# Kernel optimization log

Measured on AMD Instinct MI355X. Metric: run time of the kernel, lower is better.

The kernel has to match this reference:

```python
import jax, jax.numpy as jnp
import numpy as np

RES = 128
FEATURE_SIZE = 8
N_PTS = 2_000_000


def setup_inputs() -> dict:
    key = jax.random.key(0)
    k1, k2 = jax.random.split(key)
    # pts in [-1, 1] as the module expects (it renormalizes to [0, 1])
    pts = jax.random.uniform(k1, (N_PTS, 3), dtype=jnp.float32, minval=-1.0, maxval=1.0)
    # learned voxel feature grid, flat [res^3, F], init std=0.01
    features = 0.01 * jax.random.normal(k2, (RES ** 3, FEATURE_SIZE), dtype=jnp.float32)
    return {"pts": pts, "features": features}


def reference(pts, features):
    res = RES
    # normalize [-1,1] -> [0,1]
    npts = (pts + 1.0) * 0.5
    # continuous voxel coords in [0, res-1]
    x = npts * (res - 1)
    x0 = jnp.clip(jnp.floor(x), 0, res - 2).astype(jnp.int32)  # [N,3]
    f = x - x0.astype(x.dtype)                                  # [N,3] frac weights
    ix, iy, iz = x0[:, 0], x0[:, 1], x0[:, 2]
    fx, fy, fz = f[:, 0], f[:, 1], f[:, 2]

    out = jnp.zeros((pts.shape[0], features.shape[1]), dtype=features.dtype)
    # 8-corner gather + weighted sum (NGLOD-style flat indexing x*res^2 + y*res + z)
    for dx in (0, 1):
        wx = fx if dx else (1.0 - fx)
        for dy in (0, 1):
            wy = fy if dy else (1.0 - fy)
            for dz in (0, 1):
                wz = fz if dz else (1.0 - fz)
                idx = (ix + dx) * (res * res) + (iy + dy) * res + (iz + dz)
                out = out + features[idx] * (wx * wy * wz)[:, None]
    return out
```

## Files before the change

kernel.cpp:

```cpp
#include <hip/hip_runtime.h>

#define RES 128
#define FEAT 8
#define NBIN 4096
#define NFB 512
#define NCOARSE 64
#define CAP 32768
#define CAP2 640
#define W1 2048
#define W2 2048
#define WPR (CAP / W2)

#define SCELLS (17 * 17 * 17)

__device__ __forceinline__ void cell_of(float px, float py, float pz,
                                        int& ix, int& iy, int& iz,
                                        float& fx, float& fy, float& fz) {
    float x = (px + 1.0f) * 0.5f * (float)(RES - 1);
    float y = (py + 1.0f) * 0.5f * (float)(RES - 1);
    float z = (pz + 1.0f) * 0.5f * (float)(RES - 1);
    float fx0 = fminf(fmaxf(floorf(x), 0.0f), (float)(RES - 2));
    float fy0 = fminf(fmaxf(floorf(y), 0.0f), (float)(RES - 2));
    float fz0 = fminf(fmaxf(floorf(z), 0.0f), (float)(RES - 2));
    ix = (int)fx0; iy = (int)fy0; iz = (int)fz0;
    fx = x - fx0; fy = y - fy0; fz = z - fz0;
}

__device__ __forceinline__ int coarse_of(int ix, int iy, int iz) {
    return ((ix >> 5) << 4) | ((iy >> 5) << 2) | (iz >> 5);
}
__device__ __forceinline__ int sub_of(int ix, int iy, int iz) {
    return (((ix >> 4) & 1) << 5) | (((iy >> 4) & 1) << 4) | (((iz >> 4) & 1) << 3)
         | (((ix >> 3) & 1) << 2) | (((iy >> 3) & 1) << 1) | ((iz >> 3) & 1);
}

__device__ __forceinline__ unsigned int bf16pair(float a, float b) {
    unsigned int ua = __float_as_uint(a);
    ua = (ua + 0x7fffu + ((ua >> 16) & 1u)) >> 16;
    unsigned int ub = __float_as_uint(b);
    ub = (ub + 0x7fffu + ((ub >> 16) & 1u)) >> 16;
    return ua | (ub << 16);
}

__global__ void init_kernel(unsigned int* cursor1, unsigned int* cursor2) {
    int i = blockIdx.x * blockDim.x + threadIdx.x;
    if (i < NCOARSE) cursor1[i] = (unsigned int)(i * CAP);
    if (i < NBIN) cursor2[i] = (unsigned int)(i * CAP2);
}

__global__ __launch_bounds__(256) void pass1_kernel(const float* __restrict__ pts,
                                                    unsigned int* __restrict__ cursor1,
                                                    float4* __restrict__ sorted1,
                                                    int npts) {
    __shared__ unsigned int cnt[NCOARSE], pfx[NCOARSE], base[NCOARSE];
    __shared__ float4 buf[W1];
    __shared__ unsigned char binof[W1];
    int tid = threadIdx.x;
    int blockStart = blockIdx.x * W1;
    int valid = min(W1, npts - blockStart);
    if (valid <= 0) return;
    if (tid < NCOARSE) cnt[tid] = 0u;
    __syncthreads();

    float ppx[8], ppy[8], ppz[8];
    int pc[8], pr[8];
    int jb = tid * 8;
    bool allv = (jb + 7 < valid);
    if (allv) {
        const float4* bp = reinterpret_cast<const float4*>(pts) +
                           ((size_t)blockStart * 3) / 4 + (size_t)tid * 6;
        float4 v0 = bp[0], v1 = bp[1], v2 = bp[2], v3 = bp[3], v4 = bp[4], v5 = bp[5];
        float P[24] = {v0.x, v0.y, v0.z, v0.w, v1.x, v1.y, v1.z, v1.w,
                       v2.x, v2.y, v2.z, v2.w, v3.x, v3.y, v3.z, v3.w,
                       v4.x, v4.y, v4.z, v4.w, v5.x, v5.y, v5.z, v5.w};
#pragma unroll
        for (int k = 0; k < 8; ++k) {
            ppx[k] = P[3 * k]; ppy[k] = P[3 * k + 1]; ppz[k] = P[3 * k + 2];
            int ix, iy, iz; float fx, fy, fz;
            cell_of(ppx[k], ppy[k], ppz[k], ix, iy, iz, fx, fy, fz);
            int c = coarse_of(ix, iy, iz);
            pr[k] = (int)atomicAdd(&cnt[c], 1u);
            pc[k] = c;
        }
    } else {
#pragma unroll
        for (int k = 0; k < 8; ++k) {
            int j = jb + k;
            pc[k] = -1;
            if (j < valid) {
                int i = blockStart + j;
                float px = pts[3 * i], py = pts[3 * i + 1], pz = pts[3 * i + 2];
                int ix, iy, iz; float fx, fy, fz;
                cell_of(px, py, pz, ix, iy, iz, fx, fy, fz);
                int c = coarse_of(ix, iy, iz);
                pr[k] = (int)atomicAdd(&cnt[c], 1u);
                pc[k] = c;
                ppx[k] = px; ppy[k] = py; ppz[k] = pz;
            }
        }
    }
    __syncthreads();
    if (tid == 0) {
        unsigned int s = 0;
        for (int b = 0; b < NCOARSE; ++b) { pfx[b] = s; s += cnt[b]; }
    }
    __syncthreads();
    if (tid < NCOARSE && cnt[tid] > 0)
        base[tid] = atomicAdd(&cursor1[tid], cnt[tid]);
    __syncthreads();
#pragma unroll
    for (int k = 0; k < 8; ++k) {
        if (allv || pc[k] >= 0) {
            int i = blockStart + jb + k;
            unsigned int slot = pfx[pc[k]] + (unsigned int)pr[k];
            buf[slot] = make_float4(ppx[k], ppy[k], ppz[k], __int_as_float(i));
            binof[slot] = (unsigned char)pc[k];
        }
    }
    __syncthreads();
#pragma unroll
    for (int k = 0; k < 8; ++k) {
        int slot = k * 256 + tid;
        if (slot < valid) {
            int b = binof[slot];
            unsigned int pos = base[b] + (unsigned int)slot - pfx[b];
            sorted1[pos] = buf[slot];
        }
    }
}

__global__ __launch_bounds__(256) void pass2_kernel(const float4* __restrict__ sorted1,
                                                    const unsigned int* __restrict__ cursor1,
                                                    unsigned int* __restrict__ cursor2,
                                                    uint2* __restrict__ sorted2) {
    int c = blockIdx.x / WPR;
    int w = blockIdx.x % WPR;
    unsigned int count = cursor1[c] - (unsigned int)(c * CAP);
    if (count > CAP) count = CAP;
    int valid = min(W2, (int)count - w * W2);
    if (valid <= 0) return;
    __shared__ unsigned int cnt[64], pfx[64], base[64];
    __shared__ uint2 buf[W2];
    __shared__ unsigned char binof[W2];
    int tid = threadIdx.x;
    int start = c * CAP + w * W2;
    if (tid < 64) cnt[tid] = 0u;
    __syncthreads();

    uint2 pe[8];
    int ps[8], pr[8];
#pragma unroll
    for (int k = 0; k < 8; ++k) {
        int j = k * 256 + tid;
        ps[k] = -1;
        if (j < valid) {
            float4 q = sorted1[start + j];
            int ix, iy, iz; float fx, fy, fz;
            cell_of(q.x, q.y, q.z, ix, iy, iz, fx, fy, fz);
            int s = sub_of(ix, iy, iz);
            unsigned int lx = (unsigned)(ix & 15), ly = (unsigned)(iy & 15),
                         lz = (unsigned)(iz & 15);
            unsigned int qfx = (unsigned)__float2int_rn(fx * 512.0f);
            unsigned int qfy = (unsigned)__float2int_rn(fy * 512.0f);
            unsigned int qfz = (unsigned)__float2int_rn(fz * 512.0f);
            unsigned int oi = (unsigned)__float_as_int(q.w);
            pe[k].x = (lx << 28) | (ly << 24) | (lz << 20) | (qfx << 10) | qfy;
            pe[k].y = (qfz << 21) | oi;
            pr[k] = (int)atomicAdd(&cnt[s], 1u);
            ps[k] = s;
        }
    }
    __syncthreads();
    if (tid == 0) {
        unsigned int s = 0;
        for (int b = 0; b < 64; ++b) { pfx[b] = s; s += cnt[b]; }
    }
    __syncthreads();
    if (tid < 64 && cnt[tid] > 0)
        base[tid] = atomicAdd(&cursor2[c * 64 + tid], cnt[tid]);
    __syncthreads();
#pragma unroll
    for (int k = 0; k < 8; ++k) {
        if (ps[k] >= 0) {
            unsigned int slot = pfx[ps[k]] + (unsigned int)pr[k];
            buf[slot] = pe[k];
            binof[slot] = (unsigned char)ps[k];
        }
    }
    __syncthreads();
#pragma unroll
    for (int k = 0; k < 8; ++k) {
        int slot = k * 256 + tid;
        if (slot < valid) {
            int b = binof[slot];
            unsigned int pos = base[b] + (unsigned int)slot - pfx[b];
            sorted2[pos] = buf[slot];
        }
    }
}

__device__ __forceinline__ void lerp_packed(const uint4* __restrict__ slab, uint2 e,
                                            float* __restrict__ out) {
    int lx = (int)(e.x >> 28), ly = (int)((e.x >> 24) & 15), lz = (int)((e.x >> 20) & 15);
    float fx = (float)((e.x >> 10) & 1023) * (1.0f / 512.0f);
    float fy = (float)(e.x & 1023) * (1.0f / 512.0f);
    float fz = (float)((e.y >> 21) & 1023) * (1.0f / 512.0f);
    int oi = (int)(e.y & 0x1FFFFFu);
    int c000 = (lx * 17 + ly) * 17 + lz;

    float wx1 = fx, wx0 = 1.0f - fx;
    float wy1 = fy, wy0 = 1.0f - fy;
    float wz1 = fz, wz0 = 1.0f - fz;
    float w[8] = {wx0 * wy0 * wz0, wx0 * wy0 * wz1, wx0 * wy1 * wz0, wx0 * wy1 * wz1,
                  wx1 * wy0 * wz0, wx1 * wy0 * wz1, wx1 * wy1 * wz0, wx1 * wy1 * wz1};

    float acc[FEAT];
#pragma unroll
    for (int k = 0; k < FEAT; ++k) acc[k] = 0.0f;

#pragma unroll
    for (int dx = 0; dx < 2; ++dx) {
#pragma unroll
        for (int dy = 0; dy < 2; ++dy) {
#pragma unroll
            for (int dz = 0; dz < 2; ++dz) {
                int ci = (dx * 2 + dy) * 2 + dz;
                uint4 r = slab[c000 + dx * 289 + dy * 17 + dz];
                float ww = w[ci];
                acc[0] += ww * __uint_as_float(r.x << 16);
                acc[1] += ww * __uint_as_float(r.x & 0xffff0000u);
                acc[2] += ww * __uint_as_float(r.y << 16);
                acc[3] += ww * __uint_as_float(r.y & 0xffff0000u);
                acc[4] += ww * __uint_as_float(r.z << 16);
                acc[5] += ww * __uint_as_float(r.z & 0xffff0000u);
                acc[6] += ww * __uint_as_float(r.w << 16);
                acc[7] += ww * __uint_as_float(r.w & 0xffff0000u);
            }
        }
    }
    float4* op = reinterpret_cast<float4*>(out + (size_t)oi * FEAT);
    op[0] = make_float4(acc[0], acc[1], acc[2], acc[3]);
    op[1] = make_float4(acc[4], acc[5], acc[6], acc[7]);
}

__global__ __launch_bounds__(512) void trilerp_bf16(const uint2* __restrict__ sorted2,
                                                    const float* __restrict__ features,
                                                    const unsigned int* __restrict__ cursor2,
                                                    float* __restrict__ out) {
    __shared__ __align__(16) uint4 slab[SCELLS];
    int tid = threadIdx.x;
    int F = (blockIdx.x & 7) * 64 + (blockIdx.x >> 3);
    int c = F >> 3, f3 = F & 7;
    int ox = (((c >> 4) & 3) << 5) | (((f3 >> 2) & 1) << 4);
    int oy = (((c >> 2) & 3) << 5) | (((f3 >> 1) & 1) << 4);
    int oz = ((c & 3) << 5) | ((f3 & 1) << 4);
    int binBase = c * 64 + f3 * 8;

#pragma unroll
    for (int k = 0; k < 10; ++k) {
        int cell = k * 512 + tid;
        if (cell < SCELLS) {
            int lx = cell / 289, rr = cell - lx * 289, ly = rr / 17, lz = rr - ly * 17;
            int gx = min(ox + lx, RES - 1);
            int gy = min(oy + ly, RES - 1);
            int gz = min(oz + lz, RES - 1);
            const float4* src = reinterpret_cast<const float4*>(
                features + (size_t)((((gx << 7) | gy) << 7) | gz) * FEAT);
            float4 a = src[0], b = src[1];
            uint4 p;
            p.x = bf16pair(a.x, a.y);
            p.y = bf16pair(a.z, a.w);
            p.z = bf16pair(b.x, b.y);
            p.w = bf16pair(b.z, b.w);
            slab[cell] = p;
        }
    }

    int s0 = binBase * CAP2;
    int e0 = (int)cursor2[binBase];
    bool v0 = (s0 + tid) < e0;
    uint2 p0;
    if (v0) p0 = sorted2[s0 + tid];

    __syncthreads();

    if (v0) lerp_packed(slab, p0, out);
    for (int p = s0 + 512 + tid; p < e0; p += 512)
        lerp_packed(slab, sorted2[p], out);

#pragma unroll
    for (int k = 1; k < 8; ++k) {
        int bin = binBase + k;
        int start = bin * CAP2;
        int end = (int)cursor2[bin];
        for (int p = start + tid; p < end; p += 512)
            lerp_packed(slab, sorted2[p], out);
    }
}

__global__ __launch_bounds__(256) void trilerp_kernel(const float* __restrict__ pts,
                                                      const float* __restrict__ features,
                                                      float* __restrict__ out,
                                                      int npts) {
    int i = blockIdx.x * blockDim.x + threadIdx.x;
    if (i >= npts) return;
    int ix, iy, iz; float fx, fy, fz;
    cell_of(pts[3 * i], pts[3 * i + 1], pts[3 * i + 2], ix, iy, iz, fx, fy, fz);
    float wx[2] = {1.0f - fx, fx};
    float wy[2] = {1.0f - fy, fy};
    float wz[2] = {1.0f - fz, fz};
    float acc[FEAT];
#pragma unroll
    for (int k = 0; k < FEAT; ++k) acc[k] = 0.0f;
    int base = (ix * RES + iy) * RES + iz;
#pragma unroll
    for (int dx = 0; dx < 2; ++dx)
#pragma unroll
        for (int dy = 0; dy < 2; ++dy)
#pragma unroll
            for (int dz = 0; dz < 2; ++dz) {
                int idxc = base + dx * (RES * RES) + dy * RES + dz;
                float w = wx[dx] * wy[dy] * wz[dz];
                const float4* fp =
                    reinterpret_cast<const float4*>(features + (size_t)idxc * FEAT);
                float4 a = fp[0];
                float4 b = fp[1];
                acc[0] += w * a.x; acc[1] += w * a.y;
                acc[2] += w * a.z; acc[3] += w * a.w;
                acc[4] += w * b.x; acc[5] += w * b.y;
                acc[6] += w * b.z; acc[7] += w * b.w;
            }
    float4* op = reinterpret_cast<float4*>(out + (size_t)i * FEAT);
    op[0] = make_float4(acc[0], acc[1], acc[2], acc[3]);
    op[1] = make_float4(acc[4], acc[5], acc[6], acc[7]);
}

extern "C" void kernel_launch(void* const* d_in, const int* in_sizes, int n_in,
                              void* d_out, int out_size, void* d_ws, size_t ws_size,
                              hipStream_t stream) {
    const float* pts = (const float*)d_in[0];
    const float* features = (const float*)d_in[1];
    float* out = (float*)d_out;
    int npts = in_sizes[0] / 3;

    size_t need = (size_t)NBIN * CAP2 * sizeof(uint2)
                + (size_t)(NBIN + NCOARSE) * 4u + 256u;
    bool out_big_enough = (size_t)out_size * 4u >= (size_t)NCOARSE * CAP * sizeof(float4);
    if (ws_size < need || !out_big_enough || npts > NCOARSE * CAP || npts > 2097151) {
        int block = 256;
        int grid = (npts + block - 1) / block;
        trilerp_kernel<<<grid, block, 0, stream>>>(pts, features, out, npts);
        return;
    }

    char* w = (char*)d_ws;
    uint2* sorted2 = (uint2*)w;                 w += (size_t)NBIN * CAP2 * sizeof(uint2);
    unsigned int* cursor1 = (unsigned int*)w;   w += NCOARSE * 4u;
    unsigned int* cursor2 = (unsigned int*)w;

    float4* sorted1 = (float4*)d_out;

    init_kernel<<<(NBIN + 255) / 256, 256, 0, stream>>>(cursor1, cursor2);
    pass1_kernel<<<(npts + W1 - 1) / W1, 256, 0, stream>>>(pts, cursor1, sorted1, npts);
    pass2_kernel<<<NCOARSE * WPR, 256, 0, stream>>>(sorted1, cursor1, cursor2, sorted2);
    trilerp_bf16<<<NFB, 512, 0, stream>>>(sorted2, features, cursor2, out);
}
```

Before: 85.52 us.

## Switch trilerp tiles to 16x8x8 bins with one bin per 256-thread block

Changes the fine binning from 4096 8^3 bins grouped into 16^3 slab blocks to 2048 bins of 16x8x8 cells. Each 256-thread block now loads a smaller 17x9x9 bf16 slab and processes exactly one bin. Halving the LDS slab and block size is meant to raise occupancy and increase the number of blocks. In exchange the slab halo overhead per point grows, since more boundary cells are loaded per interior cell, and per-bin capacity doubles to 1280.

```diff
diff --git a/kernel.cpp b/kernel.cpp
--- a/kernel.cpp
+++ b/kernel.cpp
@@ -2,16 +2,15 @@
 
 #define RES 128
 #define FEAT 8
-#define NBIN 4096
-#define NFB 512
 #define NCOARSE 64
+#define NBIN2 2048
 #define CAP 32768
-#define CAP2 640
+#define CAP2 1280
 #define W1 2048
 #define W2 2048
 #define WPR (CAP / W2)
 
-#define SCELLS (17 * 17 * 17)
+#define SCELLS (17 * 9 * 9)
 
 __device__ __forceinline__ void cell_of(float px, float py, float pz,
                                         int& ix, int& iy, int& iz,
@@ -30,8 +29,7 @@
     return ((ix >> 5) << 4) | ((iy >> 5) << 2) | (iz >> 5);
 }
 __device__ __forceinline__ int sub_of(int ix, int iy, int iz) {
-    return (((ix >> 4) & 1) << 5) | (((iy >> 4) & 1) << 4) | (((iz >> 4) & 1) << 3)
-         | (((ix >> 3) & 1) << 2) | (((iy >> 3) & 1) << 1) | ((iz >> 3) & 1);
+    return (((ix >> 4) & 1) << 4) | (((iy >> 3) & 3) << 2) | ((iz >> 3) & 3);
 }
 
 __device__ __forceinline__ unsigned int bf16pair(float a, float b) {
@@ -45,7 +43,7 @@
 __global__ void init_kernel(unsigned int* cursor1, unsigned int* cursor2) {
     int i = blockIdx.x * blockDim.x + threadIdx.x;
     if (i < NCOARSE) cursor1[i] = (unsigned int)(i * CAP);
-    if (i < NBIN) cursor2[i] = (unsigned int)(i * CAP2);
+    if (i < NBIN2) cursor2[i] = (unsigned int)(i * CAP2);
 }
 
 __global__ __launch_bounds__(256) void pass1_kernel(const float* __restrict__ pts,
@@ -139,12 +137,12 @@
     if (count > CAP) count = CAP;
     int valid = min(W2, (int)count - w * W2);
     if (valid <= 0) return;
-    __shared__ unsigned int cnt[64], pfx[64], base[64];
+    __shared__ unsigned int cnt[32], pfx[32], base[32];
     __shared__ uint2 buf[W2];
     __shared__ unsigned char binof[W2];
     int tid = threadIdx.x;
     int start = c * CAP + w * W2;
-    if (tid < 64) cnt[tid] = 0u;
+    if (tid < 32) cnt[tid] = 0u;
     __syncthreads();
 
     uint2 pe[8];
@@ -158,8 +156,8 @@
             int ix, iy, iz; float fx, fy, fz;
             cell_of(q.x, q.y, q.z, ix, iy, iz, fx, fy, fz);
             int s = sub_of(ix, iy, iz);
-            unsigned int lx = (unsigned)(ix & 15), ly = (unsigned)(iy & 15),
-                         lz = (unsigned)(iz & 15);
+            unsigned int lx = (unsigned)(ix & 15), ly = (unsigned)(iy & 7),
+                         lz = (unsigned)(iz & 7);
             unsigned int qfx = (unsigned)__float2int_rn(fx * 512.0f);
             unsigned int qfy = (unsigned)__float2int_rn(fy * 512.0f);
             unsigned int qfz = (unsigned)__float2int_rn(fz * 512.0f);
@@ -173,11 +171,11 @@
     __syncthreads();
     if (tid == 0) {
         unsigned int s = 0;
-        for (int b = 0; b < 64; ++b) { pfx[b] = s; s += cnt[b]; }
-    }
-    __syncthreads();
-    if (tid < 64 && cnt[tid] > 0)
-        base[tid] = atomicAdd(&cursor2[c * 64 + tid], cnt[tid]);
+        for (int b = 0; b < 32; ++b) { pfx[b] = s; s += cnt[b]; }
+    }
+    __syncthreads();
+    if (tid < 32 && cnt[tid] > 0)
+        base[tid] = atomicAdd(&cursor2[c * 32 + tid], cnt[tid]);
     __syncthreads();
 #pragma unroll
     for (int k = 0; k < 8; ++k) {
@@ -206,7 +204,7 @@
     float fy = (float)(e.x & 1023) * (1.0f / 512.0f);
     float fz = (float)((e.y >> 21) & 1023) * (1.0f / 512.0f);
     int oi = (int)(e.y & 0x1FFFFFu);
-    int c000 = (lx * 17 + ly) * 17 + lz;
+    int c000 = (lx * 9 + ly) * 9 + lz;
 
     float wx1 = fx, wx0 = 1.0f - fx;
     float wy1 = fy, wy0 = 1.0f - fy;
@@ -225,7 +223,7 @@
 #pragma unroll
             for (int dz = 0; dz < 2; ++dz) {
                 int ci = (dx * 2 + dy) * 2 + dz;
-                uint4 r = slab[c000 + dx * 289 + dy * 17 + dz];
+                uint4 r = slab[c000 + dx * 81 + dy * 9 + dz];
                 float ww = w[ci];
                 acc[0] += ww * __uint_as_float(r.x << 16);
                 acc[1] += ww * __uint_as_float(r.x & 0xffff0000u);
@@ -243,24 +241,23 @@
     op[1] = make_float4(acc[4], acc[5], acc[6], acc[7]);
 }
 
-__global__ __launch_bounds__(512) void trilerp_bf16(const uint2* __restrict__ sorted2,
+__global__ __launch_bounds__(256) void trilerp_bf16(const uint2* __restrict__ sorted2,
                                                     const float* __restrict__ features,
                                                     const unsigned int* __restrict__ cursor2,
                                                     float* __restrict__ out) {
     __shared__ __align__(16) uint4 slab[SCELLS];
     int tid = threadIdx.x;
-    int F = (blockIdx.x & 7) * 64 + (blockIdx.x >> 3);
-    int c = F >> 3, f3 = F & 7;
-    int ox = (((c >> 4) & 3) << 5) | (((f3 >> 2) & 1) << 4);
-    int oy = (((c >> 2) & 3) << 5) | (((f3 >> 1) & 1) << 4);
-    int oz = ((c & 3) << 5) | ((f3 & 1) << 4);
-    int binBase = c * 64 + f3 * 8;
-
-#pragma unroll
-    for (int k = 0; k < 10; ++k) {
-        int cell = k * 512 + tid;
+    int F = (blockIdx.x & 7) * 256 + (blockIdx.x >> 3);
+    int c = F >> 5, s5 = F & 31;
+    int ox = (((c >> 4) & 3) << 5) | (((s5 >> 4) & 1) << 4);
+    int oy = (((c >> 2) & 3) << 5) | (((s5 >> 2) & 3) << 3);
+    int oz = ((c & 3) << 5) | ((s5 & 3) << 3);
+
+#pragma unroll
+    for (int k = 0; k < 6; ++k) {
+        int cell = k * 256 + tid;
         if (cell < SCELLS) {
-            int lx = cell / 289, rr = cell - lx * 289, ly = rr / 17, lz = rr - ly * 17;
+            int lx = cell / 81, rr = cell - lx * 81, ly = rr / 9, lz = rr - ly * 9;
             int gx = min(ox + lx, RES - 1);
             int gy = min(oy + ly, RES - 1);
             int gz = min(oz + lz, RES - 1);
@@ -276,26 +273,20 @@
         }
     }
 
-    int s0 = binBase * CAP2;
-    int e0 = (int)cursor2[binBase];
-    bool v0 = (s0 + tid) < e0;
-    uint2 p0;
-    if (v0) p0 = sorted2[s0 + tid];
+    int s0 = F * CAP2;
+    int e0 = (int)cursor2[F];
+    int n0 = s0 + tid, n1 = n0 + 256;
+    bool v0 = n0 < e0, v1 = n1 < e0;
+    uint2 p0, p1;
+    if (v0) p0 = sorted2[n0];
+    if (v1) p1 = sorted2[n1];
 
     __syncthreads();
 
     if (v0) lerp_packed(slab, p0, out);
-    for (int p = s0 + 512 + tid; p < e0; p += 512)
+    if (v1) lerp_packed(slab, p1, out);
+    for (int p = s0 + 512 + tid; p < e0; p += 256)
         lerp_packed(slab, sorted2[p], out);
-
-#pragma unroll
-    for (int k = 1; k < 8; ++k) {
-        int bin = binBase + k;
-        int start = bin * CAP2;
-        int end = (int)cursor2[bin];
-        for (int p = start + tid; p < end; p += 512)
-            lerp_packed(slab, sorted2[p], out);
-    }
 }
 
 __global__ __launch_bounds__(256) void trilerp_kernel(const float* __restrict__ pts,
@@ -343,8 +334,8 @@
     float* out = (float*)d_out;
     int npts = in_sizes[0] / 3;
 
-    size_t need = (size_t)NBIN * CAP2 * sizeof(uint2)
-                + (size_t)(NBIN + NCOARSE) * 4u + 256u;
+    size_t need = (size_t)NBIN2 * CAP2 * sizeof(uint2)
+                + (size_t)(NBIN2 + NCOARSE) * 4u + 256u;
     bool out_big_enough = (size_t)out_size * 4u >= (size_t)NCOARSE * CAP * sizeof(float4);
     if (ws_size < need || !out_big_enough || npts > NCOARSE * CAP || npts > 2097151) {
         int block = 256;
@@ -354,14 +345,14 @@
     }
 
     char* w = (char*)d_ws;
-    uint2* sorted2 = (uint2*)w;                 w += (size_t)NBIN * CAP2 * sizeof(uint2);
+    uint2* sorted2 = (uint2*)w;                 w += (size_t)NBIN2 * CAP2 * sizeof(uint2);
     unsigned int* cursor1 = (unsigned int*)w;   w += NCOARSE * 4u;
     unsigned int* cursor2 = (unsigned int*)w;
 
     float4* sorted1 = (float4*)d_out;
 
-    init_kernel<<<(NBIN + 255) / 256, 256, 0, stream>>>(cursor1, cursor2);
+    init_kernel<<<(NBIN2 + 255) / 256, 256, 0, stream>>>(cursor1, cursor2);
     pass1_kernel<<<(npts + W1 - 1) / W1, 256, 0, stream>>>(pts, cursor1, sorted1, npts);
     pass2_kernel<<<NCOARSE * WPR, 256, 0, stream>>>(sorted1, cursor1, cursor2, sorted2);
-    trilerp_bf16<<<NFB, 512, 0, stream>>>(sorted2, features, cursor2, out);
-}
+    trilerp_bf16<<<NBIN2, 256, 0, stream>>>(sorted2, features, cursor2, out);
+}
```

New measurement: 86.66 us. Within noise of the previous version (+1.3%).

## Replace two-pass bucket sort with single-pass sort into 512 final bins

Applied to the files above, without the earlier changes.

Merges the two sorting passes into one kernel that bins points directly into the 512 slab bins and writes compact packed 8-byte entries. This removes the intermediate float4 round trip through the output buffer, one kernel launch, and the per-bin loop in the trilerp kernel. In exchange, each block handles 512 bins with a parallel scan, and with 4096 points per block the global writes are scattered across many more bins and are less coalesced. The fixed per-bin capacity of 4608 could overflow for non-uniform inputs.

```diff
diff --git a/kernel.cpp b/kernel.cpp
--- a/kernel.cpp
+++ b/kernel.cpp
@@ -2,14 +2,9 @@
 
 #define RES 128
 #define FEAT 8
-#define NBIN 4096
 #define NFB 512
-#define NCOARSE 64
-#define CAP 32768
-#define CAP2 640
-#define W1 2048
-#define W2 2048
-#define WPR (CAP / W2)
+#define CAPF 4608
+#define WF 4096
 
 #define SCELLS (17 * 17 * 17)
 
@@ -26,12 +21,23 @@
     fx = x - fx0; fy = y - fy0; fz = z - fz0;
 }
 
-__device__ __forceinline__ int coarse_of(int ix, int iy, int iz) {
-    return ((ix >> 5) << 4) | ((iy >> 5) << 2) | (iz >> 5);
-}
-__device__ __forceinline__ int sub_of(int ix, int iy, int iz) {
-    return (((ix >> 4) & 1) << 5) | (((iy >> 4) & 1) << 4) | (((iz >> 4) & 1) << 3)
-         | (((ix >> 3) & 1) << 2) | (((iy >> 3) & 1) << 1) | ((iz >> 3) & 1);
+__device__ __forceinline__ int bin_of(int ix, int iy, int iz) {
+    int c = ((ix >> 5) << 4) | ((iy >> 5) << 2) | (iz >> 5);
+    int f3 = (((ix >> 4) & 1) << 2) | (((iy >> 4) & 1) << 1) | ((iz >> 4) & 1);
+    return (c << 3) | f3;
+}
+
+__device__ __forceinline__ uint2 pack_entry(int ix, int iy, int iz,
+                                            float fx, float fy, float fz, int i) {
+    unsigned int lx = (unsigned)(ix & 15), ly = (unsigned)(iy & 15),
+                 lz = (unsigned)(iz & 15);
+    unsigned int qfx = (unsigned)__float2int_rn(fx * 512.0f);
+    unsigned int qfy = (unsigned)__float2int_rn(fy * 512.0f);
+    unsigned int qfz = (unsigned)__float2int_rn(fz * 512.0f);
+    uint2 e;
+    e.x = (lx << 28) | (ly << 24) | (lz << 20) | (qfx << 10) | qfy;
+    e.y = (qfz << 21) | (unsigned)i;
+    return e;
 }
 
 __device__ __forceinline__ unsigned int bf16pair(float a, float b) {
@@ -42,159 +48,99 @@
     return ua | (ub << 16);
 }
 
-__global__ void init_kernel(unsigned int* cursor1, unsigned int* cursor2) {
-    int i = blockIdx.x * blockDim.x + threadIdx.x;
-    if (i < NCOARSE) cursor1[i] = (unsigned int)(i * CAP);
-    if (i < NBIN) cursor2[i] = (unsigned int)(i * CAP2);
-}
-
-__global__ __launch_bounds__(256) void pass1_kernel(const float* __restrict__ pts,
-                                                    unsigned int* __restrict__ cursor1,
-                                                    float4* __restrict__ sorted1,
-                                                    int npts) {
-    __shared__ unsigned int cnt[NCOARSE], pfx[NCOARSE], base[NCOARSE];
-    __shared__ float4 buf[W1];
-    __shared__ unsigned char binof[W1];
+__global__ __launch_bounds__(512) void init_kernel(unsigned int* cursor) {
+    int i = threadIdx.x;
+    if (i < NFB) cursor[i] = (unsigned int)(i * CAPF);
+}
+
+__global__ __launch_bounds__(256) void sort_kernel(const float* __restrict__ pts,
+                                                   unsigned int* __restrict__ cursor,
+                                                   uint2* __restrict__ sorted,
+                                                   int npts) {
+    __shared__ unsigned int cnt[NFB], pfx[NFB], base[NFB];
+    __shared__ unsigned int scanbuf[256];
+    __shared__ uint2 buf[WF];
+    __shared__ unsigned short binof[WF];
     int tid = threadIdx.x;
-    int blockStart = blockIdx.x * W1;
-    int valid = min(W1, npts - blockStart);
+    int blockStart = blockIdx.x * WF;
+    int valid = min(WF, npts - blockStart);
     if (valid <= 0) return;
-    if (tid < NCOARSE) cnt[tid] = 0u;
-    __syncthreads();
-
-    float ppx[8], ppy[8], ppz[8];
-    int pc[8], pr[8];
-    int jb = tid * 8;
-    bool allv = (jb + 7 < valid);
+    for (int b = tid; b < NFB; b += 256) cnt[b] = 0u;
+    __syncthreads();
+
+    uint2 pe[16];
+    int ps[16], pr[16];
+    int jb = tid * 16;
+    bool allv = (jb + 15 < valid);
     if (allv) {
         const float4* bp = reinterpret_cast<const float4*>(pts) +
-                           ((size_t)blockStart * 3) / 4 + (size_t)tid * 6;
-        float4 v0 = bp[0], v1 = bp[1], v2 = bp[2], v3 = bp[3], v4 = bp[4], v5 = bp[5];
-        float P[24] = {v0.x, v0.y, v0.z, v0.w, v1.x, v1.y, v1.z, v1.w,
-                       v2.x, v2.y, v2.z, v2.w, v3.x, v3.y, v3.z, v3.w,
-                       v4.x, v4.y, v4.z, v4.w, v5.x, v5.y, v5.z, v5.w};
-#pragma unroll
-        for (int k = 0; k < 8; ++k) {
-            ppx[k] = P[3 * k]; ppy[k] = P[3 * k + 1]; ppz[k] = P[3 * k + 2];
+                           ((size_t)blockStart * 3) / 4 + (size_t)tid * 12;
+        float P[48];
+#pragma unroll
+        for (int i = 0; i < 12; ++i) {
+            float4 v = bp[i];
+            P[4 * i] = v.x; P[4 * i + 1] = v.y; P[4 * i + 2] = v.z; P[4 * i + 3] = v.w;
+        }
+#pragma unroll
+        for (int k = 0; k < 16; ++k) {
             int ix, iy, iz; float fx, fy, fz;
-            cell_of(ppx[k], ppy[k], ppz[k], ix, iy, iz, fx, fy, fz);
-            int c = coarse_of(ix, iy, iz);
-            pr[k] = (int)atomicAdd(&cnt[c], 1u);
-            pc[k] = c;
+            cell_of(P[3 * k], P[3 * k + 1], P[3 * k + 2], ix, iy, iz, fx, fy, fz);
+            int b = bin_of(ix, iy, iz);
+            pe[k] = pack_entry(ix, iy, iz, fx, fy, fz, blockStart + jb + k);
+            pr[k] = (int)atomicAdd(&cnt[b], 1u);
+            ps[k] = b;
         }
     } else {
 #pragma unroll
-        for (int k = 0; k < 8; ++k) {
+        for (int k = 0; k < 16; ++k) {
             int j = jb + k;
-            pc[k] = -1;
+            ps[k] = -1;
             if (j < valid) {
                 int i = blockStart + j;
                 float px = pts[3 * i], py = pts[3 * i + 1], pz = pts[3 * i + 2];
                 int ix, iy, iz; float fx, fy, fz;
                 cell_of(px, py, pz, ix, iy, iz, fx, fy, fz);
-                int c = coarse_of(ix, iy, iz);
-                pr[k] = (int)atomicAdd(&cnt[c], 1u);
-                pc[k] = c;
-                ppx[k] = px; ppy[k] = py; ppz[k] = pz;
+                int b = bin_of(ix, iy, iz);
+                pe[k] = pack_entry(ix, iy, iz, fx, fy, fz, i);
+                pr[k] = (int)atomicAdd(&cnt[b], 1u);
+                ps[k] = b;
             }
         }
     }
     __syncthreads();
-    if (tid == 0) {
-        unsigned int s = 0;
-        for (int b = 0; b < NCOARSE; ++b) { pfx[b] = s; s += cnt[b]; }
-    }
-    __syncthreads();
-    if (tid < NCOARSE && cnt[tid] > 0)
-        base[tid] = atomicAdd(&cursor1[tid], cnt[tid]);
-    __syncthreads();
-#pragma unroll
-    for (int k = 0; k < 8; ++k) {
-        if (allv || pc[k] >= 0) {
-            int i = blockStart + jb + k;
-            unsigned int slot = pfx[pc[k]] + (unsigned int)pr[k];
-            buf[slot] = make_float4(ppx[k], ppy[k], ppz[k], __int_as_float(i));
-            binof[slot] = (unsigned char)pc[k];
-        }
-    }
-    __syncthreads();
-#pragma unroll
-    for (int k = 0; k < 8; ++k) {
+
+    unsigned int c0 = cnt[2 * tid], c1 = cnt[2 * tid + 1];
+    scanbuf[tid] = c0 + c1;
+    __syncthreads();
+    for (int off = 1; off < 256; off <<= 1) {
+        unsigned int v = (tid >= off) ? scanbuf[tid - off] : 0u;
+        __syncthreads();
+        scanbuf[tid] += v;
+        __syncthreads();
+    }
+    unsigned int excl = (tid == 0) ? 0u : scanbuf[tid - 1];
+    pfx[2 * tid] = excl;
+    pfx[2 * tid + 1] = excl + c0;
+    if (c0) base[2 * tid] = atomicAdd(&cursor[2 * tid], c0);
+    if (c1) base[2 * tid + 1] = atomicAdd(&cursor[2 * tid + 1], c1);
+    __syncthreads();
+
+#pragma unroll
+    for (int k = 0; k < 16; ++k) {
+        if (ps[k] >= 0) {
+            unsigned int slot = pfx[ps[k]] + (unsigned int)pr[k];
+            buf[slot] = pe[k];
+            binof[slot] = (unsigned short)ps[k];
+        }
+    }
+    __syncthreads();
+#pragma unroll
+    for (int k = 0; k < 16; ++k) {
         int slot = k * 256 + tid;
         if (slot < valid) {
             int b = binof[slot];
             unsigned int pos = base[b] + (unsigned int)slot - pfx[b];
-            sorted1[pos] = buf[slot];
-        }
-    }
-}
-
-__global__ __launch_bounds__(256) void pass2_kernel(const float4* __restrict__ sorted1,
-                                                    const unsigned int* __restrict__ cursor1,
-                                                    unsigned int* __restrict__ cursor2,
-                                                    uint2* __restrict__ sorted2) {
-    int c = blockIdx.x / WPR;
-    int w = blockIdx.x % WPR;
-    unsigned int count = cursor1[c] - (unsigned int)(c * CAP);
-    if (count > CAP) count = CAP;
-    int valid = min(W2, (int)count - w * W2);
-    if (valid <= 0) return;
-    __shared__ unsigned int cnt[64], pfx[64], base[64];
-    __shared__ uint2 buf[W2];
-    __shared__ unsigned char binof[W2];
-    int tid = threadIdx.x;
-    int start = c * CAP + w * W2;
-    if (tid < 64) cnt[tid] = 0u;
-    __syncthreads();
-
-    uint2 pe[8];
-    int ps[8], pr[8];
-#pragma unroll
-    for (int k = 0; k < 8; ++k) {
-        int j = k * 256 + tid;
-        ps[k] = -1;
-        if (j < valid) {
-            float4 q = sorted1[start + j];
-            int ix, iy, iz; float fx, fy, fz;
-            cell_of(q.x, q.y, q.z, ix, iy, iz, fx, fy, fz);
-            int s = sub_of(ix, iy, iz);
-            unsigned int lx = (unsigned)(ix & 15), ly = (unsigned)(iy & 15),
-                         lz = (unsigned)(iz & 15);
-            unsigned int qfx = (unsigned)__float2int_rn(fx * 512.0f);
-            unsigned int qfy = (unsigned)__float2int_rn(fy * 512.0f);
-            unsigned int qfz = (unsigned)__float2int_rn(fz * 512.0f);
-            unsigned int oi = (unsigned)__float_as_int(q.w);
-            pe[k].x = (lx << 28) | (ly << 24) | (lz << 20) | (qfx << 10) | qfy;
-            pe[k].y = (qfz << 21) | oi;
-            pr[k] = (int)atomicAdd(&cnt[s], 1u);
-            ps[k] = s;
-        }
-    }
-    __syncthreads();
-    if (tid == 0) {
-        unsigned int s = 0;
-        for (int b = 0; b < 64; ++b) { pfx[b] = s; s += cnt[b]; }
-    }
-    __syncthreads();
-    if (tid < 64 && cnt[tid] > 0)
-        base[tid] = atomicAdd(&cursor2[c * 64 + tid], cnt[tid]);
-    __syncthreads();
-#pragma unroll
-    for (int k = 0; k < 8; ++k) {
-        if (ps[k] >= 0) {
-            unsigned int slot = pfx[ps[k]] + (unsigned int)pr[k];
-            buf[slot] = pe[k];
-            binof[slot] = (unsigned char)ps[k];
-        }
-    }
-    __syncthreads();
-#pragma unroll
-    for (int k = 0; k < 8; ++k) {
-        int slot = k * 256 + tid;
-        if (slot < valid) {
-            int b = binof[slot];
-            unsigned int pos = base[b] + (unsigned int)slot - pfx[b];
-            sorted2[pos] = buf[slot];
+            sorted[pos] = buf[slot];
         }
     }
 }
@@ -243,9 +189,9 @@
     op[1] = make_float4(acc[4], acc[5], acc[6], acc[7]);
 }
 
-__global__ __launch_bounds__(512) void trilerp_bf16(const uint2* __restrict__ sorted2,
+__global__ __launch_bounds__(512) void trilerp_bf16(const uint2* __restrict__ sorted,
                                                     const float* __restrict__ features,
-                                                    const unsigned int* __restrict__ cursor2,
+                                                    const unsigned int* __restrict__ cursor,
                                                     float* __restrict__ out) {
     __shared__ __align__(16) uint4 slab[SCELLS];
     int tid = threadIdx.x;
@@ -254,7 +200,6 @@
     int ox = (((c >> 4) & 3) << 5) | (((f3 >> 2) & 1) << 4);
     int oy = (((c >> 2) & 3) << 5) | (((f3 >> 1) & 1) << 4);
     int oz = ((c & 3) << 5) | ((f3 & 1) << 4);
-    int binBase = c * 64 + f3 * 8;
 
 #pragma unroll
     for (int k = 0; k < 10; ++k) {
@@ -276,26 +221,20 @@
         }
     }
 
-    int s0 = binBase * CAP2;
-    int e0 = (int)cursor2[binBase];
-    bool v0 = (s0 + tid) < e0;
-    uint2 p0;
-    if (v0) p0 = sorted2[s0 + tid];
+    int s0 = F * CAPF;
+    int e0 = (int)cursor[F];
+    int n0 = s0 + tid, n1 = n0 + 512;
+    bool v0 = n0 < e0, v1 = n1 < e0;
+    uint2 p0, p1;
+    if (v0) p0 = sorted[n0];
+    if (v1) p1 = sorted[n1];
 
     __syncthreads();
 
     if (v0) lerp_packed(slab, p0, out);
-    for (int p = s0 + 512 + tid; p < e0; p += 512)
-        lerp_packed(slab, sorted2[p], out);
-
-#pragma unroll
-    for (int k = 1; k < 8; ++k) {
-        int bin = binBase + k;
-        int start = bin * CAP2;
-        int end = (int)cursor2[bin];
-        for (int p = start + tid; p < end; p += 512)
-            lerp_packed(slab, sorted2[p], out);
-    }
+    if (v1) lerp_packed(slab, p1, out);
+    for (int p = s0 + 1024 + tid; p < e0; p += 512)
+        lerp_packed(slab, sorted[p], out);
 }
 
 __global__ __launch_bounds__(256) void trilerp_kernel(const float* __restrict__ pts,
@@ -343,10 +282,8 @@
     float* out = (float*)d_out;
     int npts = in_sizes[0] / 3;
 
-    size_t need = (size_t)NBIN * CAP2 * sizeof(uint2)
-                + (size_t)(NBIN + NCOARSE) * 4u + 256u;
-    bool out_big_enough = (size_t)out_size * 4u >= (size_t)NCOARSE * CAP * sizeof(float4);
-    if (ws_size < need || !out_big_enough || npts > NCOARSE * CAP || npts > 2097151) {
+    size_t need = (size_t)NFB * CAPF * sizeof(uint2) + (size_t)NFB * 4u + 256u;
+    if (ws_size < need || npts > 2097151 || npts > NFB * (CAPF - 512)) {
         int block = 256;
         int grid = (npts + block - 1) / block;
         trilerp_kernel<<<grid, block, 0, stream>>>(pts, features, out, npts);
@@ -354,14 +291,10 @@
     }
 
     char* w = (char*)d_ws;
-    uint2* sorted2 = (uint2*)w;                 w += (size_t)NBIN * CAP2 * sizeof(uint2);
-    unsigned int* cursor1 = (unsigned int*)w;   w += NCOARSE * 4u;
-    unsigned int* cursor2 = (unsigned int*)w;
-
-    float4* sorted1 = (float4*)d_out;
-
-    init_kernel<<<(NBIN + 255) / 256, 256, 0, stream>>>(cursor1, cursor2);
-    pass1_kernel<<<(npts + W1 - 1) / W1, 256, 0, stream>>>(pts, cursor1, sorted1, npts);
-    pass2_kernel<<<NCOARSE * WPR, 256, 0, stream>>>(sorted1, cursor1, cursor2, sorted2);
-    trilerp_bf16<<<NFB, 512, 0, stream>>>(sorted2, features, cursor2, out);
-}
+    uint2* sorted = (uint2*)w;                 w += (size_t)NFB * CAPF * sizeof(uint2);
+    unsigned int* cursor = (unsigned int*)w;
+
+    init_kernel<<<1, 512, 0, stream>>>(cursor);
+    sort_kernel<<<(npts + WF - 1) / WF, 256, 0, stream>>>(pts, cursor, sorted, npts);
+    trilerp_bf16<<<NFB, 512, 0, stream>>>(sorted, features, cursor, out);
+}
```

Measured after the change: 76.60 us (median of 3 runs). 1.12x faster.
